# Performance work log

Hardware: AMD Instinct MI355X
Metric: run time of the kernel (lower is better)

Reference implementation:

```python
import jax, jax.numpy as jnp
import numpy as np
import math

B, D_MODEL, EMB, ORDER, SEQ = 4, 64, 33, 64, 256
TARGET, FAST_PCT, SLOW_PCT = 0.01, 0.3, 1.5


def _pos_emb(L, emb_dim):
    # PositionalEmbedding: t in [0,1], complex exponential bands
    t = jnp.linspace(0.0, 1.0, L)[None, :, None]                     # [1,L,1]
    bands = (emb_dim - 1) // 2
    t_r = jnp.linspace(0.0, L - 1.0, L)[None, :, None]
    w = 2.0 * math.pi * t_r / L
    f = jnp.linspace(1e-4, bands - 1.0, bands)[None, None]
    zc = jnp.exp(-1j * f * w)
    z = jnp.concatenate([t, zc.real, zc.imag], axis=-1)              # [1,L,emb_dim]
    return z.astype(jnp.float32), t.astype(jnp.float32)


def setup_inputs() -> dict:
    key = jax.random.key(0)
    ks = jax.random.split(key, 24)
    z, _ = _pos_emb(SEQ, EMB)

    def lin(k, fan_in, fan_out):
        return jax.random.normal(k, (fan_in, fan_out), jnp.float32) / np.sqrt(fan_in)

    inp = {
        'x': jax.random.normal(ks[0], (B, D_MODEL, SEQ, SEQ), jnp.float32),
        'z': z,
        'Xw1': lin(ks[1], EMB, ORDER), 'Xb1': jax.random.normal(ks[2], (ORDER,), jnp.float32) * 0.02,
        'Xw2': lin(ks[3], ORDER, ORDER), 'Xb2': jax.random.normal(ks[4], (ORDER,), jnp.float32) * 0.02,
        'Xw3': lin(ks[5], ORDER, ORDER), 'Xb3': jax.random.normal(ks[6], (ORDER,), jnp.float32) * 0.02,
        'Xwo': lin(ks[7], ORDER, D_MODEL),
        'Xfreq': jnp.ones((1, ORDER), jnp.float32),  # Sin freq, w=1, shared across layers
        'Yw1': lin(ks[8], EMB, ORDER), 'Yb1': jax.random.normal(ks[9], (ORDER,), jnp.float32) * 0.02,
        'Yw2': lin(ks[10], ORDER, ORDER), 'Yb2': jax.random.normal(ks[11], (ORDER,), jnp.float32) * 0.02,
        'Yw3': lin(ks[12], ORDER, ORDER), 'Yb3': jax.random.normal(ks[13], (ORDER,), jnp.float32) * 0.02,
        'Ywo': lin(ks[14], ORDER, D_MODEL),
        'Yfreq': jnp.ones((1, ORDER), jnp.float32),
        'bias': jax.random.normal(ks[15], (D_MODEL,), jnp.float32),
        'L': SEQ,
    }
    return inp


def _implicit_filter(z, w1, b1, w2, b2, w3, b3, wo, freq, t, deltas):
    # MLP with shared Sin activation, then exponential modulation (shift=0)
    h = jnp.sin(freq * (z @ w1 + b1))
    h = jnp.sin(freq * (h @ w2 + b2))
    h = jnp.sin(freq * (h @ w3 + b3))
    h = h @ wo                                   # [1,L,d_model]
    decay = jnp.exp(-t * jnp.abs(deltas))        # [1,L,d_model]
    return h * decay


def reference(x, z, Xw1, Xb1, Xw2, Xb2, Xw3, Xb3, Xwo, Xfreq,
              Yw1, Yb1, Yw2, Yb2, Yw3, Yb3, Ywo, Yfreq, bias, L):
    d_model = x.shape[1]
    t = jnp.linspace(0.0, 1.0, L)[None, :, None].astype(jnp.float32)
    max_dec = math.log(TARGET) / FAST_PCT
    min_dec = math.log(TARGET) / SLOW_PCT
    deltas = jnp.linspace(min_dec, max_dec, d_model)[None, None].astype(jnp.float32)

    hx = _implicit_filter(z, Xw1, Xb1, Xw2, Xb2, Xw3, Xb3, Xwo, Xfreq, t, deltas)
    hy = _implicit_filter(z, Yw1, Yb1, Yw2, Yb2, Yw3, Yb3, Ywo, Yfreq, t, deltas)
    # separable outer-product 2D kernel: [1,L,L,d_model] -> [d_model,L,L]
    k = jnp.einsum('ijk,imk->ijmk', hx, hy)[0]
    k = jnp.transpose(k, (2, 0, 1))

    fft_size = 2 * L
    k_f = jnp.fft.rfft2(k, s=(fft_size, fft_size)) / fft_size       # [D, 2L, L+1]
    u_f = jnp.fft.rfft2(x.astype(jnp.float32), s=(fft_size, fft_size))  # [B, D, 2L, L+1]
    y = jnp.fft.irfft2(u_f * k_f, s=(fft_size, fft_size))[..., :L, :L]
    out = y + x * bias[:, None, None]
    return out.astype(x.dtype)
```

## Files before the change

### kernel.cpp

```cpp
#include <hip/hip_runtime.h>

#define SL 256

typedef _Float16 f16;
typedef _Float16 f16x8 __attribute__((ext_vector_type(8)));
typedef _Float16 f16x4 __attribute__((ext_vector_type(4)));
typedef float f32x4 __attribute__((ext_vector_type(4)));

__global__ __launch_bounds__(64) void k_filters(
    const float* __restrict__ z,
    const float* __restrict__ Xw1, const float* __restrict__ Xb1,
    const float* __restrict__ Xw2, const float* __restrict__ Xb2,
    const float* __restrict__ Xw3, const float* __restrict__ Xb3,
    const float* __restrict__ Xwo, const float* __restrict__ Xfreq,
    const float* __restrict__ Yw1, const float* __restrict__ Yb1,
    const float* __restrict__ Yw2, const float* __restrict__ Yb2,
    const float* __restrict__ Yw3, const float* __restrict__ Yb3,
    const float* __restrict__ Ywo, const float* __restrict__ Yfreq,
    float* __restrict__ hx, float* __restrict__ hy)
{
    const int l = blockIdx.x;
    const int sel = blockIdx.y;
    const int t = threadIdx.x;
    const float* w1 = sel ? Yw1 : Xw1;  const float* b1 = sel ? Yb1 : Xb1;
    const float* w2 = sel ? Yw2 : Xw2;  const float* b2 = sel ? Yb2 : Xb2;
    const float* w3 = sel ? Yw3 : Xw3;  const float* b3 = sel ? Yb3 : Xb3;
    const float* wo = sel ? Ywo : Xwo;  const float* freq = sel ? Yfreq : Xfreq;
    float* hout = sel ? hy : hx;

    __shared__ float zb[33];
    __shared__ float ha[64];
    __shared__ float hb[64];

    if (t < 33) zb[t] = z[l * 33 + t];
    __syncthreads();

    const float fr = freq[t];
    float s = b1[t];
    for (int k = 0; k < 33; ++k) s += zb[k] * w1[k * 64 + t];
    ha[t] = sinf(fr * s);
    __syncthreads();

    s = b2[t];
    for (int k = 0; k < 64; ++k) s += ha[k] * w2[k * 64 + t];
    hb[t] = sinf(fr * s);
    __syncthreads();

    s = b3[t];
    for (int k = 0; k < 64; ++k) s += hb[k] * w3[k * 64 + t];
    ha[t] = sinf(fr * s);
    __syncthreads();

    s = 0.f;
    for (int k = 0; k < 64; ++k) s += ha[k] * wo[k * 64 + t];

    const float MIN_DEC = -3.0701134573253937f;
    const float MAX_DEC = -15.350567286626968f;
    float ad = fabsf(MIN_DEC + (MAX_DEC - MIN_DEC) * ((float)t / 63.0f));
    float tl = (float)l / 255.0f;
    hout[l * 64 + t] = s * expf(-tl * ad);
}

__device__ __forceinline__ void build_R(f16* R, const float* __restrict__ hcol,
                                        int d, int tid)
{
    for (int idx = tid; idx < 8 * 520; idx += 512) {
        int c = idx / 520;
        int k = idx - c * 520;
        int u = k + c;
        float v = (u <= 255) ? hcol[(255 - u) * 64 + d] : 0.f;
        R[idx] = (f16)v;
    }
}

__global__ __launch_bounds__(512, 2) void k_fused(
    const float* __restrict__ x, const float* __restrict__ hx,
    const float* __restrict__ hy, const float* __restrict__ bias,
    float* __restrict__ out)
{
    const int bd = blockIdx.x;
    const int d  = bd & 63;
    const int tid  = threadIdx.x;
    const int lane = tid & 63;
    const int wave = tid >> 6;
    const int ln   = lane & 15;
    const int quad = lane >> 4;

    __shared__ __align__(16) f16 tmp[256 * 256];
    __shared__ __align__(16) f16 R[8 * 520];

    const float* xbd = x + (size_t)bd * (SL * SL);

    build_R(R, hy, d, tid);

    f32x4 acc[32];
#pragma unroll
    for (int a = 0; a < 32; ++a) acc[a] = (f32x4){0.f, 0.f, 0.f, 0.f};

    __syncthreads();

    {
        const int wp = wave & 3;
        const int wj = wave >> 2;
        for (int q0 = 0; q0 < 256; q0 += 32) {
            f16x8 af[4], bf[8];
#pragma unroll
            for (int rt = 0; rt < 4; ++rt) {
                int p = wp * 64 + rt * 16 + ln;
                const float* src = xbd + p * SL + q0 + quad * 8;
                float4 v0 = *(const float4*)src;
                float4 v1 = *(const float4*)(src + 4);
                f16x8 h;
                h[0] = (f16)v0.x; h[1] = (f16)v0.y; h[2] = (f16)v0.z; h[3] = (f16)v0.w;
                h[4] = (f16)v1.x; h[5] = (f16)v1.y; h[6] = (f16)v1.z; h[7] = (f16)v1.w;
                af[rt] = h;
            }
#pragma unroll
            for (int ct = 0; ct < 8; ++ct) {
                int j = wj * 128 + ct * 16 + ln;
                int s0 = 255 - j + q0 + quad * 8;
                int c = s0 & 7;
                bf[ct] = *(const f16x8*)&R[c * 520 + (s0 - c)];
            }
#pragma unroll
            for (int rt = 0; rt < 4; ++rt)
#pragma unroll
                for (int ct = 0; ct < 8; ++ct)
                    acc[rt * 8 + ct] = __builtin_amdgcn_mfma_f32_16x16x32_f16(
                        af[rt], bf[ct], acc[rt * 8 + ct], 0, 0, 0);
        }

#pragma unroll
        for (int rt = 0; rt < 4; ++rt)
#pragma unroll
            for (int ct = 0; ct < 8; ++ct) {
                int j = wj * 128 + ct * 16 + ln;
                int pb = wp * 64 + rt * 16 + quad * 4;
                f32x4 a = acc[rt * 8 + ct];
                f16x4 v;
                v[0] = (f16)a[0]; v[1] = (f16)a[1];
                v[2] = (f16)a[2]; v[3] = (f16)a[3];
                *(f16x4*)&tmp[j * 256 + (pb ^ ((j & 7) << 3))] = v;
            }
    }

    __syncthreads();
    build_R(R, hx, d, tid);
#pragma unroll
    for (int a = 0; a < 32; ++a) acc[a] = (f32x4){0.f, 0.f, 0.f, 0.f};
    __syncthreads();

    const int wi  = wave & 1;
    const int wj2 = wave >> 1;
    for (int p0 = 0; p0 < 256; p0 += 32) {
        f16x8 af[8], bf[4];
#pragma unroll
        for (int rt = 0; rt < 8; ++rt) {
            int i = wi * 128 + rt * 16 + ln;
            int s0 = 255 - i + p0 + quad * 8;
            int c = s0 & 7;
            af[rt] = *(const f16x8*)&R[c * 520 + (s0 - c)];
        }
#pragma unroll
        for (int ct = 0; ct < 4; ++ct) {
            int j = wj2 * 64 + ct * 16 + ln;
            int off = (p0 + quad * 8) ^ ((j & 7) << 3);
            bf[ct] = *(const f16x8*)&tmp[j * 256 + off];
        }
#pragma unroll
        for (int rt = 0; rt < 8; ++rt)
#pragma unroll
            for (int ct = 0; ct < 4; ++ct)
                acc[rt * 4 + ct] = __builtin_amdgcn_mfma_f32_16x16x32_f16(
                    af[rt], bf[ct], acc[rt * 4 + ct], 0, 0, 0);
    }

    const float bv = bias[d];
    const float sc = 1.0f / 512.0f;
    float* obd = out + (size_t)bd * (SL * SL);
#pragma unroll
    for (int rt = 0; rt < 8; ++rt)
#pragma unroll
        for (int ct = 0; ct < 4; ++ct) {
            int j  = wj2 * 64 + ct * 16 + ln;
            int ib = wi * 128 + rt * 16 + quad * 4;
            f32x4 a = acc[rt * 4 + ct];
#pragma unroll
            for (int r = 0; r < 4; ++r) {
                int i = ib + r;
                obd[i * SL + j] = a[r] * sc + xbd[i * SL + j] * bv;
            }
        }
}

extern "C" void kernel_launch(void* const* d_in, const int* in_sizes, int n_in,
                              void* d_out, int out_size, void* d_ws, size_t ws_size,
                              hipStream_t stream)
{
    (void)in_sizes; (void)n_in; (void)out_size; (void)ws_size;
    const float* x     = (const float*)d_in[0];
    const float* z     = (const float*)d_in[1];
    const float* Xw1   = (const float*)d_in[2];
    const float* Xb1   = (const float*)d_in[3];
    const float* Xw2   = (const float*)d_in[4];
    const float* Xb2   = (const float*)d_in[5];
    const float* Xw3   = (const float*)d_in[6];
    const float* Xb3   = (const float*)d_in[7];
    const float* Xwo   = (const float*)d_in[8];
    const float* Xfreq = (const float*)d_in[9];
    const float* Yw1   = (const float*)d_in[10];
    const float* Yb1   = (const float*)d_in[11];
    const float* Yw2   = (const float*)d_in[12];
    const float* Yb2   = (const float*)d_in[13];
    const float* Yw3   = (const float*)d_in[14];
    const float* Yb3   = (const float*)d_in[15];
    const float* Ywo   = (const float*)d_in[16];
    const float* Yfreq = (const float*)d_in[17];
    const float* bias  = (const float*)d_in[18];

    float* hx = (float*)d_ws;
    float* hy = hx + 256 * 64;

    k_filters<<<dim3(256, 2), 64, 0, stream>>>(
        z, Xw1, Xb1, Xw2, Xb2, Xw3, Xb3, Xwo, Xfreq,
        Yw1, Yb1, Yw2, Yb2, Yw3, Yb3, Ywo, Yfreq, hx, hy);
    k_fused<<<256, 512, 0, stream>>>(x, hx, hy, bias, (float*)d_out);
}
```

Baseline: 195.3 us.

## Use 1024-thread blocks with smaller per-wave tiles, prefetch x, vectorize epilogue

Doubles k_fused block size to 16 waves, halving each wave's MFMA tile so accumulators drop from 32 to 16 vectors. The first GEMM now software-prefetches the next x chunk into registers while computing the current one. The second GEMM swaps its operands so each lane writes a contiguous float4 of output and reads x as a float4, replacing scalar strided stores. The aims are more latency hiding and wider global accesses. The cost is more waves per block and a launch bound that may force register spills; 64KB+ of shared memory per block still caps residency at one block per CU.

```diff
diff --git a/kernel.cpp b/kernel.cpp
--- a/kernel.cpp
+++ b/kernel.cpp
@@ -64,7 +64,7 @@
 __device__ __forceinline__ void build_R(f16* R, const float* __restrict__ hcol,
                                         int d, int tid)
 {
-    for (int idx = tid; idx < 8 * 520; idx += 512) {
+    for (int idx = tid; idx < 8 * 520; idx += 1024) {
         int c = idx / 520;
         int k = idx - c * 520;
         int u = k + c;
@@ -73,7 +73,7 @@
     }
 }
 
-__global__ __launch_bounds__(512, 2) void k_fused(
+__global__ __launch_bounds__(1024, 4) void k_fused(
     const float* __restrict__ x, const float* __restrict__ hx,
     const float* __restrict__ hy, const float* __restrict__ bias,
     float* __restrict__ out)
@@ -93,31 +93,47 @@
 
     build_R(R, hy, d, tid);
 
-    f32x4 acc[32];
-#pragma unroll
-    for (int a = 0; a < 32; ++a) acc[a] = (f32x4){0.f, 0.f, 0.f, 0.f};
+    f32x4 acc[16];
+#pragma unroll
+    for (int a = 0; a < 16; ++a) acc[a] = (f32x4){0.f, 0.f, 0.f, 0.f};
 
     __syncthreads();
 
     {
         const int wp = wave & 3;
         const int wj = wave >> 2;
+
+        float4 pv0[4], pv1[4];
+#pragma unroll
+        for (int rt = 0; rt < 4; ++rt) {
+            const float* src = xbd + (wp * 64 + rt * 16 + ln) * SL + quad * 8;
+            pv0[rt] = *(const float4*)src;
+            pv1[rt] = *(const float4*)(src + 4);
+        }
+
         for (int q0 = 0; q0 < 256; q0 += 32) {
-            f16x8 af[4], bf[8];
+            f16x8 af[4], bf[4];
 #pragma unroll
             for (int rt = 0; rt < 4; ++rt) {
-                int p = wp * 64 + rt * 16 + ln;
-                const float* src = xbd + p * SL + q0 + quad * 8;
-                float4 v0 = *(const float4*)src;
-                float4 v1 = *(const float4*)(src + 4);
                 f16x8 h;
-                h[0] = (f16)v0.x; h[1] = (f16)v0.y; h[2] = (f16)v0.z; h[3] = (f16)v0.w;
-                h[4] = (f16)v1.x; h[5] = (f16)v1.y; h[6] = (f16)v1.z; h[7] = (f16)v1.w;
+                h[0] = (f16)pv0[rt].x; h[1] = (f16)pv0[rt].y;
+                h[2] = (f16)pv0[rt].z; h[3] = (f16)pv0[rt].w;
+                h[4] = (f16)pv1[rt].x; h[5] = (f16)pv1[rt].y;
+                h[6] = (f16)pv1[rt].z; h[7] = (f16)pv1[rt].w;
                 af[rt] = h;
             }
-#pragma unroll
-            for (int ct = 0; ct < 8; ++ct) {
-                int j = wj * 128 + ct * 16 + ln;
+            if (q0 < 224) {
+#pragma unroll
+                for (int rt = 0; rt < 4; ++rt) {
+                    const float* src = xbd + (wp * 64 + rt * 16 + ln) * SL
+                                     + q0 + 32 + quad * 8;
+                    pv0[rt] = *(const float4*)src;
+                    pv1[rt] = *(const float4*)(src + 4);
+                }
+            }
+#pragma unroll
+            for (int ct = 0; ct < 4; ++ct) {
+                int j = wj * 64 + ct * 16 + ln;
                 int s0 = 255 - j + q0 + quad * 8;
                 int c = s0 & 7;
                 bf[ct] = *(const f16x8*)&R[c * 520 + (s0 - c)];
@@ -125,18 +141,18 @@
 #pragma unroll
             for (int rt = 0; rt < 4; ++rt)
 #pragma unroll
-                for (int ct = 0; ct < 8; ++ct)
-                    acc[rt * 8 + ct] = __builtin_amdgcn_mfma_f32_16x16x32_f16(
-                        af[rt], bf[ct], acc[rt * 8 + ct], 0, 0, 0);
+                for (int ct = 0; ct < 4; ++ct)
+                    acc[rt * 4 + ct] = __builtin_amdgcn_mfma_f32_16x16x32_f16(
+                        af[rt], bf[ct], acc[rt * 4 + ct], 0, 0, 0);
         }
 
 #pragma unroll
         for (int rt = 0; rt < 4; ++rt)
 #pragma unroll
-            for (int ct = 0; ct < 8; ++ct) {
-                int j = wj * 128 + ct * 16 + ln;
+            for (int ct = 0; ct < 4; ++ct) {
+                int j = wj * 64 + ct * 16 + ln;
                 int pb = wp * 64 + rt * 16 + quad * 4;
-                f32x4 a = acc[rt * 8 + ct];
+                f32x4 a = acc[rt * 4 + ct];
                 f16x4 v;
                 v[0] = (f16)a[0]; v[1] = (f16)a[1];
                 v[2] = (f16)a[2]; v[3] = (f16)a[3];
@@ -147,28 +163,28 @@
     __syncthreads();
     build_R(R, hx, d, tid);
 #pragma unroll
-    for (int a = 0; a < 32; ++a) acc[a] = (f32x4){0.f, 0.f, 0.f, 0.f};
-    __syncthreads();
-
-    const int wi  = wave & 1;
-    const int wj2 = wave >> 1;
+    for (int a = 0; a < 16; ++a) acc[a] = (f32x4){0.f, 0.f, 0.f, 0.f};
+    __syncthreads();
+
+    const int wii = wave & 3;
+    const int wjj = wave >> 2;
     for (int p0 = 0; p0 < 256; p0 += 32) {
-        f16x8 af[8], bf[4];
-#pragma unroll
-        for (int rt = 0; rt < 8; ++rt) {
-            int i = wi * 128 + rt * 16 + ln;
+        f16x8 af[4], bf[4];
+#pragma unroll
+        for (int rt = 0; rt < 4; ++rt) {
+            int j = wjj * 64 + rt * 16 + ln;
+            int off = (p0 + quad * 8) ^ ((j & 7) << 3);
+            af[rt] = *(const f16x8*)&tmp[j * 256 + off];
+        }
+#pragma unroll
+        for (int ct = 0; ct < 4; ++ct) {
+            int i = wii * 64 + ct * 16 + ln;
             int s0 = 255 - i + p0 + quad * 8;
             int c = s0 & 7;
-            af[rt] = *(const f16x8*)&R[c * 520 + (s0 - c)];
-        }
-#pragma unroll
-        for (int ct = 0; ct < 4; ++ct) {
-            int j = wj2 * 64 + ct * 16 + ln;
-            int off = (p0 + quad * 8) ^ ((j & 7) << 3);
-            bf[ct] = *(const f16x8*)&tmp[j * 256 + off];
-        }
-#pragma unroll
-        for (int rt = 0; rt < 8; ++rt)
+            bf[ct] = *(const f16x8*)&R[c * 520 + (s0 - c)];
+        }
+#pragma unroll
+        for (int rt = 0; rt < 4; ++rt)
 #pragma unroll
             for (int ct = 0; ct < 4; ++ct)
                 acc[rt * 4 + ct] = __builtin_amdgcn_mfma_f32_16x16x32_f16(
@@ -179,17 +195,19 @@
     const float sc = 1.0f / 512.0f;
     float* obd = out + (size_t)bd * (SL * SL);
 #pragma unroll
-    for (int rt = 0; rt < 8; ++rt)
+    for (int rt = 0; rt < 4; ++rt)
 #pragma unroll
         for (int ct = 0; ct < 4; ++ct) {
-            int j  = wj2 * 64 + ct * 16 + ln;
-            int ib = wi * 128 + rt * 16 + quad * 4;
+            int i  = wii * 64 + ct * 16 + ln;
+            int jb = wjj * 64 + rt * 16 + quad * 4;
             f32x4 a = acc[rt * 4 + ct];
-#pragma unroll
-            for (int r = 0; r < 4; ++r) {
-                int i = ib + r;
-                obd[i * SL + j] = a[r] * sc + xbd[i * SL + j] * bv;
-            }
+            float4 xv = *(const float4*)(xbd + i * SL + jb);
+            float4 o;
+            o.x = a[0] * sc + xv.x * bv;
+            o.y = a[1] * sc + xv.y * bv;
+            o.z = a[2] * sc + xv.z * bv;
+            o.w = a[3] * sc + xv.w * bv;
+            *(float4*)(obd + i * SL + jb) = o;
         }
 }
 
@@ -224,5 +242,5 @@
     k_filters<<<dim3(256, 2), 64, 0, stream>>>(
         z, Xw1, Xb1, Xw2, Xb2, Xw3, Xb3, Xwo, Xfreq,
         Yw1, Yb1, Yw2, Yb2, Yw3, Yb3, Ywo, Yfreq, hx, hy);
-    k_fused<<<256, 512, 0, stream>>>(x, hx, hy, bias, (float*)d_out);
-}
+    k_fused<<<256, 1024, 0, stream>>>(x, hx, hy, bias, (float*)d_out);
+}
```

After: 192.4 us. Within noise of the previous version (-1.5%).
